# Kernel optimization log

Hardware: AMD Instinct MI355X
Metric: run time of the kernel (lower is better)

The kernel has to match this reference:

```python
import jax, jax.numpy as jnp
import numpy as np

EPS = 2.220446049250313e-16  # sys.float_info.epsilon
H_BW = 0.1  # bandwidth h


def setup_inputs() -> dict:
    key = jax.random.key(0)
    k1, k2 = jax.random.split(key)
    X = jax.random.normal(k1, (4, 256, 64, 64), dtype=jnp.float32)
    Y = jax.random.normal(k2, (4, 256, 64, 64), dtype=jnp.float32)
    return {"X_features": X, "Y_features": Y}


def _l2_normalize_c(f):
    # torch.norm(f, 2, dim=1, keepdim=True) + eps over channel dim of NCHW
    n = jnp.sqrt(jnp.sum(f * f, axis=1, keepdims=True)) + EPS
    return f / n


def reference(X_features, Y_features):
    B, C = X_features.shape[0], X_features.shape[1]
    # PONO centering: mean over channel dim of Y
    y_mean = jnp.mean(Y_features, axis=1, keepdims=True)  # [B,1,H,W]
    X = X_features - y_mean
    Y = Y_features - y_mean
    Xn = _l2_normalize_c(X).reshape(B, C, -1)  # [B,C,M]
    Yn = _l2_normalize_c(Y).reshape(B, C, -1)  # [B,C,M]
    # cosine distance matrix [B,M,M]
    d = 1.0 - jnp.einsum('bci,bcj->bij', Xn, Yn)
    d_norm = d / (jnp.min(d, axis=-1, keepdims=True) + 0.001)
    w = jnp.exp((1.0 - d_norm) / H_BW)
    A_ij = w / jnp.sum(w, axis=-1, keepdims=True)
    CX = jnp.mean(jnp.max(A_ij, axis=-1), axis=1)  # [B]
    return jnp.mean(-jnp.log(CX))
```

## Files before the change

### kernel.cpp

```cpp
#include <hip/hip_runtime.h>
#include <hip/hip_bf16.h>

typedef unsigned short u16;
typedef unsigned int u32;
typedef __attribute__((ext_vector_type(8))) __bf16 bf16x8;
typedef __attribute__((ext_vector_type(4))) float f32x4;
typedef __attribute__((ext_vector_type(8))) short short8;

#define EPSF 2.220446049250313e-16f

__device__ __forceinline__ u16 f2bf(float f) {
    u32 u = __float_as_uint(f);
    return (u16)((u + 0x7FFFu + ((u >> 16) & 1u)) >> 16);
}

__device__ __forceinline__ void gll16(const void* g, void* l) {
    __builtin_amdgcn_global_load_lds(
        (const __attribute__((address_space(1))) unsigned int*)g,
        (__attribute__((address_space(3))) unsigned int*)l, 16, 0, 0);
}

#define MEMFENCE asm volatile("" ::: "memory")
#define BAR() do { MEMFENCE; __builtin_amdgcn_s_barrier(); MEMFENCE; } while (0)
#define VMWAIT(N) do { asm volatile("s_waitcnt vmcnt(" #N ")" ::: "memory"); \
                       __builtin_amdgcn_sched_barrier(0); } while (0)

__global__ __launch_bounds__(512) void prep_kernel(
    const float* __restrict__ X, const float* __restrict__ Y,
    u16* __restrict__ XnT, u16* __restrict__ YnT)
{
    const int b  = blockIdx.x >> 7;
    const int p0 = (blockIdx.x & 127) << 5;
    const int t  = threadIdx.x;
    const int w  = t >> 6, l = t & 63;
    const size_t base = (size_t)b * 256 * 4096 + p0;

    __shared__ float TXf[32][260], TYf[32][260];
    __shared__ float part[8][16][8];
    __shared__ float meanL[32], rxL[32], ryL[32];

    const int pxp = t & 15;
    const int cs  = t >> 4;
    float sx0=0,sxx0=0,sy0=0,syy0=0, sx1=0,sxx1=0,sy1=0,syy1=0;
    #pragma unroll
    for (int k = 0; k < 8; ++k) {
        int c = cs * 8 + k;
        size_t off = base + (size_t)c * 4096 + pxp * 2;
        float2 vx = *(const float2*)(X + off);
        float2 vy = *(const float2*)(Y + off);
        TXf[pxp*2][c] = vx.x; TXf[pxp*2+1][c] = vx.y;
        TYf[pxp*2][c] = vy.x; TYf[pxp*2+1][c] = vy.y;
        sx0 += vx.x; sxx0 += vx.x*vx.x; sy0 += vy.x; syy0 += vy.x*vy.x;
        sx1 += vx.y; sxx1 += vx.y*vx.y; sy1 += vy.y; syy1 += vy.y*vy.y;
    }
    #pragma unroll
    for (int sh = 16; sh <= 32; sh <<= 1) {
        sx0 += __shfl_xor(sx0, sh, 64); sxx0 += __shfl_xor(sxx0, sh, 64);
        sy0 += __shfl_xor(sy0, sh, 64); syy0 += __shfl_xor(syy0, sh, 64);
        sx1 += __shfl_xor(sx1, sh, 64); sxx1 += __shfl_xor(sxx1, sh, 64);
        sy1 += __shfl_xor(sy1, sh, 64); syy1 += __shfl_xor(syy1, sh, 64);
    }
    if (l < 16) {
        part[w][l][0]=sx0; part[w][l][1]=sxx0; part[w][l][2]=sy0; part[w][l][3]=syy0;
        part[w][l][4]=sx1; part[w][l][5]=sxx1; part[w][l][6]=sy1; part[w][l][7]=syy1;
    }
    __syncthreads();
    if (t < 32) {
        const int pp = t >> 1, sub = (t & 1) * 4;
        float Sx=0, Sxx=0, Sy=0, Syy=0;
        #pragma unroll
        for (int ww = 0; ww < 8; ++ww) {
            Sx += part[ww][pp][sub+0]; Sxx += part[ww][pp][sub+1];
            Sy += part[ww][pp][sub+2]; Syy += part[ww][pp][sub+3];
        }
        float m = Sy * (1.f / 256.f);
        float ssx = fmaxf(Sxx - 2.f*m*Sx + 256.f*m*m, 0.f);
        float ssy = fmaxf(Syy - 2.f*m*Sy + 256.f*m*m, 0.f);
        meanL[t] = m;
        rxL[t] = 1.f / (sqrtf(ssx) + EPSF);
        ryL[t] = 1.f / (sqrtf(ssy) + EPSF);
    }
    __syncthreads();
    {
        const int c16 = t & 15, px = t >> 4;
        const float m = meanL[px], rxv = rxL[px], ryv = ryL[px];
        size_t ob = ((size_t)b * 4096 + p0 + px) * 256 + c16 * 16;
        #pragma unroll
        for (int h = 0; h < 2; ++h) {
            short8 hx, hy;
            #pragma unroll
            for (int k = 0; k < 8; ++k) {
                int c = c16 * 16 + h * 8 + k;
                hx[k] = (short)f2bf((TXf[px][c] - m) * rxv);
                hy[k] = (short)f2bf((TYf[px][c] - m) * ryv);
            }
            *(short8*)(XnT + ob + h * 8) = hx;
            *(short8*)(YnT + ob + h * 8) = hy;
        }
    }
}

template <int PASS>
__global__ __launch_bounds__(512, 2) void cx_pass(
    const u16* __restrict__ XnT, const u16* __restrict__ YnT,
    const float* __restrict__ smax, float* __restrict__ partials)
{
    __shared__ u16 As[2][2][128 * 64];
    __shared__ u16 Bs[2][2][128 * 64];
    __shared__ float red[256][4];
    __shared__ float smx[256];

    const int t = threadIdx.x;
    const int w = t >> 6;
    const int l = t & 63;
    const int wr  = w >> 2;
    const int wcn = w & 3;

    const int id   = blockIdx.x;
    const int xcd  = id & 7;
    const int slot = id >> 3;
    const int b    = xcd >> 1;
    const int tile = ((xcd & 1) << 7) | slot;
    const int it = tile >> 4, jt = tile & 15;
    const int i0 = it << 8, j0 = jt << 8;

    const u16* Ab = XnT + ((size_t)b * 4096 + i0) * 256;
    const u16* Bb = YnT + ((size_t)b * 4096 + j0) * 256;

    if (PASS == 1 && t < 256)
        smx[t] = smax[(size_t)b * 4096 + i0 + t];

    const int srow = t >> 3;
    const int sOff = srow * 256 + (((t & 7) ^ (srow & 7)) << 3);

    auto stageA = [&](int d, int h, int kt) {
        gll16(Ab + h * 32768 +         kt * 64 + sOff, &As[d][h][w * 512]);
        gll16(Ab + h * 32768 + 16384 + kt * 64 + sOff, &As[d][h][4096 + w * 512]);
    };
    auto stageB = [&](int d, int h, int kt) {
        gll16(Bb + h * 32768 +         kt * 64 + sOff, &Bs[d][h][w * 512]);
        gll16(Bb + h * 32768 + 16384 + kt * 64 + sOff, &Bs[d][h][4096 + w * 512]);
    };

    bf16x8 a[4][2], b0[2][2], b1[2][2];
    f32x4 acc[8][4] = {};

    const int l15 = l & 15;
    const int kbh = (l >> 4) << 4;

    auto readA = [&](int d, int mh) {
        const char* basep = (const char*)&As[d][wr][0];
        #pragma unroll
        for (int fm = 0; fm < 4; ++fm)
            #pragma unroll
            for (int ks = 0; ks < 2; ++ks) {
                int row = mh * 64 + fm * 16 + l15;
                int kb = ks * 64 + kbh;
                a[fm][ks] = *(const bf16x8*)(basep + row * 128 + (kb ^ ((row & 7) << 4)));
            }
    };
    auto readB = [&](int d, int nh, bf16x8 (&bb)[2][2]) {
        const char* basep = (const char*)&Bs[d][wcn >> 1][0];
        #pragma unroll
        for (int fp = 0; fp < 2; ++fp)
            #pragma unroll
            for (int ks = 0; ks < 2; ++ks) {
                int row = (wcn & 1) * 64 + (nh * 2 + fp) * 16 + l15;
                int kb = ks * 64 + kbh;
                bb[fp][ks] = *(const bf16x8*)(basep + row * 128 + (kb ^ ((row & 7) << 4)));
            }
    };
    auto mmaQ = [&](int mh, int nh, bf16x8 (&bb)[2][2]) {
        __builtin_amdgcn_s_setprio(1);
        #pragma unroll
        for (int fm = 0; fm < 4; ++fm)
            #pragma unroll
            for (int fp = 0; fp < 2; ++fp)
                #pragma unroll
                for (int ks = 0; ks < 2; ++ks)
                    acc[mh*4+fm][nh*2+fp] = __builtin_amdgcn_mfma_f32_16x16x32_bf16(
                        a[fm][ks], bb[fp][ks], acc[mh*4+fm][nh*2+fp], 0, 0, 0);
        __builtin_amdgcn_s_setprio(0);
    };

    stageA(0,0,0); stageA(0,1,0); stageB(0,0,0); stageB(0,1,0);
    stageA(1,0,1); stageA(1,1,1); stageB(1,0,1); stageB(1,1,1);

    VMWAIT(8); BAR();
    readA(0,0); readB(0,0,b0);  BAR(); mmaQ(0,0,b0);
    readB(0,1,b1);              BAR(); mmaQ(0,1,b1);
    readA(0,1);                 BAR(); mmaQ(1,1,b1);
    stageB(0,0,2);              BAR(); mmaQ(1,0,b0);
    VMWAIT(2); BAR();
    readA(1,0); readB(1,0,b0); stageB(0,1,2); BAR(); mmaQ(0,0,b0);
    readB(1,1,b1);             stageA(0,0,2); BAR(); mmaQ(0,1,b1);
    readA(1,1);                stageA(0,1,2); BAR(); mmaQ(1,1,b1);
    stageB(1,0,3);                            BAR(); mmaQ(1,0,b0);
    VMWAIT(2); BAR();
    readA(0,0); readB(0,0,b0); stageB(1,1,3); BAR(); mmaQ(0,0,b0);
    readB(0,1,b1);             stageA(1,0,3); BAR(); mmaQ(0,1,b1);
    readA(0,1);                stageA(1,1,3); BAR(); mmaQ(1,1,b1);
    BAR(); mmaQ(1,0,b0);
    VMWAIT(0); BAR();
    readA(1,0); readB(1,0,b0);  BAR(); mmaQ(0,0,b0);
    readB(1,1,b1);              BAR(); mmaQ(0,1,b1);
    readA(1,1);                 BAR(); mmaQ(1,1,b1);
    BAR(); mmaQ(1,0,b0);

    const int g = l >> 4;
    #pragma unroll
    for (int fm = 0; fm < 8; ++fm) {
        #pragma unroll
        for (int r = 0; r < 4; ++r) {
            const int rowL = wr * 128 + fm * 16 + g * 4 + r;
            float v;
            if (PASS == 0) {
                v = fmaxf(fmaxf(acc[fm][0][r], acc[fm][1][r]),
                          fmaxf(acc[fm][2][r], acc[fm][3][r]));
                v = fmaxf(v, __shfl_xor(v, 1, 64));
                v = fmaxf(v, __shfl_xor(v, 2, 64));
                v = fmaxf(v, __shfl_xor(v, 4, 64));
                v = fmaxf(v, __shfl_xor(v, 8, 64));
            } else {
                float mrow = smx[rowL];
                float itau = 1.0f / (0.1f * (1.001f - mrow));
                v = __expf((acc[fm][0][r] - mrow) * itau)
                  + __expf((acc[fm][1][r] - mrow) * itau)
                  + __expf((acc[fm][2][r] - mrow) * itau)
                  + __expf((acc[fm][3][r] - mrow) * itau);
                v += __shfl_xor(v, 1, 64);
                v += __shfl_xor(v, 2, 64);
                v += __shfl_xor(v, 4, 64);
                v += __shfl_xor(v, 8, 64);
            }
            if (l15 == 0) red[rowL][wcn] = v;
        }
    }
    BAR();
    if (t < 256) {
        float4 vv = *(const float4*)&red[t][0];
        float res = (PASS == 0)
            ? fmaxf(fmaxf(vv.x, vv.y), fmaxf(vv.z, vv.w))
            : (vv.x + vv.y) + (vv.z + vv.w);
        partials[((size_t)b * 4096 + i0 + t) * 16 + jt] = res;
    }
}

template <int OP>
__global__ __launch_bounds__(256) void reduce_rows(
    const float* __restrict__ part, float* __restrict__ outv)
{
    const int row = blockIdx.x * 256 + threadIdx.x;
    const float4* p = (const float4*)(part + (size_t)row * 16);
    float a = (OP == 0) ? -2.0f : 0.0f;
    #pragma unroll
    for (int k = 0; k < 4; ++k) {
        float4 v = p[k];
        if (OP == 0) a = fmaxf(a, fmaxf(fmaxf(v.x, v.y), fmaxf(v.z, v.w)));
        else         a += (v.x + v.y) + (v.z + v.w);
    }
    outv[row] = a;
}

__global__ __launch_bounds__(1024) void final_kernel(
    const float* __restrict__ Stot, float* __restrict__ out)
{
    __shared__ float red[16];
    const int t = threadIdx.x;
    float loss = 0.f;
    for (int b = 0; b < 4; ++b) {
        float s = 0.f;
        #pragma unroll
        for (int k = 0; k < 4; ++k)
            s += 1.0f / Stot[(size_t)b * 4096 + k * 1024 + t];
        #pragma unroll
        for (int sh = 1; sh <= 32; sh <<= 1) s += __shfl_xor(s, sh, 64);
        if ((t & 63) == 0) red[t >> 6] = s;
        __syncthreads();
        if (t == 0) {
            float tot = 0.f;
            #pragma unroll
            for (int k = 0; k < 16; ++k) tot += red[k];
            loss += -logf(tot * (1.f / 4096.f));
        }
        __syncthreads();
    }
    if (t == 0) out[0] = loss * 0.25f;
}

extern "C" void kernel_launch(void* const* d_in, const int* in_sizes, int n_in,
                              void* d_out, int out_size, void* d_ws, size_t ws_size,
                              hipStream_t stream)
{
    const float* X = (const float*)d_in[0];
    const float* Y = (const float*)d_in[1];
    char* ws = (char*)d_ws;
    u16* XnT = (u16*)(ws);
    u16* YnT = (u16*)(ws + (8u << 20));
    float* partials = (float*)(ws + (16u << 20));
    float* smax = (float*)(ws + (17u << 20));
    float* Stot = (float*)(ws + (17u << 20) + (64u << 10));
    float* out = (float*)d_out;

    hipLaunchKernelGGL(prep_kernel, dim3(512), dim3(512), 0, stream,
                       X, Y, XnT, YnT);
    hipLaunchKernelGGL((cx_pass<0>), dim3(1024), dim3(512), 0, stream,
                       XnT, YnT, smax, partials);
    hipLaunchKernelGGL((reduce_rows<0>), dim3(64), dim3(256), 0, stream,
                       partials, smax);
    hipLaunchKernelGGL((cx_pass<1>), dim3(1024), dim3(512), 0, stream,
                       XnT, YnT, smax, partials);
    hipLaunchKernelGGL((reduce_rows<1>), dim3(64), dim3(256), 0, stream,
                       partials, Stot);
    hipLaunchKernelGGL(final_kernel, dim3(1), dim3(1024), 0, stream, Stot, out);
}
```

Baseline: 200.5 us.

## Restructure CX passes into A-in-register tiles streaming long B row ranges

Each cx_pass block now keeps its 128-row A slice entirely in registers and streams 1024 B rows through a double-buffered LDS tile, accumulating the row max or exp-sum across the whole range. This cuts the column-tile partial count from 16 to 4, shrinks reduce_rows, and uses exp2 with a precomputed FMA offset. The prep kernel also gets odd-stride LDS padding and a remapped write pattern to reduce bank conflicts. The risks are higher register pressure from holding A fragments, fewer and smaller blocks (512 of 256 threads), and lower MFMA density per B load.

```diff
diff --git a/kernel.cpp b/kernel.cpp
--- a/kernel.cpp
+++ b/kernel.cpp
@@ -35,7 +35,7 @@
     const int w  = t >> 6, l = t & 63;
     const size_t base = (size_t)b * 256 * 4096 + p0;
 
-    __shared__ float TXf[32][260], TYf[32][260];
+    __shared__ float TXf[32 * 261], TYf[32 * 261];
     __shared__ float part[8][16][8];
     __shared__ float meanL[32], rxL[32], ryL[32];
 
@@ -48,8 +48,8 @@
         size_t off = base + (size_t)c * 4096 + pxp * 2;
         float2 vx = *(const float2*)(X + off);
         float2 vy = *(const float2*)(Y + off);
-        TXf[pxp*2][c] = vx.x; TXf[pxp*2+1][c] = vx.y;
-        TYf[pxp*2][c] = vy.x; TYf[pxp*2+1][c] = vy.y;
+        TXf[(pxp*2) * 261 + c] = vx.x; TXf[(pxp*2+1) * 261 + c] = vx.y;
+        TYf[(pxp*2) * 261 + c] = vy.x; TYf[(pxp*2+1) * 261 + c] = vy.y;
         sx0 += vx.x; sxx0 += vx.x*vx.x; sy0 += vy.x; syy0 += vy.x*vy.x;
         sx1 += vx.y; sxx1 += vx.y*vx.y; sy1 += vy.y; syy1 += vy.y*vy.y;
     }
@@ -82,17 +82,17 @@
     }
     __syncthreads();
     {
-        const int c16 = t & 15, px = t >> 4;
+        const int px = t & 31, cb = t >> 5;
         const float m = meanL[px], rxv = rxL[px], ryv = ryL[px];
-        size_t ob = ((size_t)b * 4096 + p0 + px) * 256 + c16 * 16;
+        size_t ob = ((size_t)b * 4096 + p0 + px) * 256 + cb * 16;
         #pragma unroll
         for (int h = 0; h < 2; ++h) {
             short8 hx, hy;
             #pragma unroll
             for (int k = 0; k < 8; ++k) {
-                int c = c16 * 16 + h * 8 + k;
-                hx[k] = (short)f2bf((TXf[px][c] - m) * rxv);
-                hy[k] = (short)f2bf((TYf[px][c] - m) * ryv);
+                int c = cb * 16 + h * 8 + k;
+                hx[k] = (short)f2bf((TXf[px * 261 + c] - m) * rxv);
+                hy[k] = (short)f2bf((TYf[px * 261 + c] - m) * ryv);
             }
             *(short8*)(XnT + ob + h * 8) = hx;
             *(short8*)(YnT + ob + h * 8) = hy;
@@ -101,149 +101,135 @@
 }
 
 template <int PASS>
-__global__ __launch_bounds__(512, 2) void cx_pass(
+__global__ __launch_bounds__(256, 2) void cx_pass(
     const u16* __restrict__ XnT, const u16* __restrict__ YnT,
     const float* __restrict__ smax, float* __restrict__ partials)
 {
-    __shared__ u16 As[2][2][128 * 64];
-    __shared__ u16 Bs[2][2][128 * 64];
-    __shared__ float red[256][4];
-    __shared__ float smx[256];
+    __shared__ u16 Bs[2][16384];
 
     const int t = threadIdx.x;
     const int w = t >> 6;
     const int l = t & 63;
-    const int wr  = w >> 2;
-    const int wcn = w & 3;
+    const int l15 = l & 15, g = l >> 4;
 
     const int id   = blockIdx.x;
     const int xcd  = id & 7;
     const int slot = id >> 3;
     const int b    = xcd >> 1;
-    const int tile = ((xcd & 1) << 7) | slot;
-    const int it = tile >> 4, jt = tile & 15;
-    const int i0 = it << 8, j0 = jt << 8;
+    const int tid2 = ((xcd & 1) << 6) | slot;
+    const int it = tid2 >> 2, jr = tid2 & 3;
+    const int i0 = it << 7;
+    const int j0 = jr << 10;
 
     const u16* Ab = XnT + ((size_t)b * 4096 + i0) * 256;
     const u16* Bb = YnT + ((size_t)b * 4096 + j0) * 256;
 
-    if (PASS == 1 && t < 256)
-        smx[t] = smax[(size_t)b * 4096 + i0 + t];
-
-    const int srow = t >> 3;
-    const int sOff = srow * 256 + (((t & 7) ^ (srow & 7)) << 3);
-
-    auto stageA = [&](int d, int h, int kt) {
-        gll16(Ab + h * 32768 +         kt * 64 + sOff, &As[d][h][w * 512]);
-        gll16(Ab + h * 32768 + 16384 + kt * 64 + sOff, &As[d][h][4096 + w * 512]);
+    bf16x8 a[2][8];
+    #pragma unroll
+    for (int fm = 0; fm < 2; ++fm)
+        #pragma unroll
+        for (int ks = 0; ks < 8; ++ks)
+            a[fm][ks] = *(const bf16x8*)((const char*)Ab +
+                (size_t)(w * 32 + fm * 16 + l15) * 512 + ks * 64 + g * 16);
+
+    float moff[2][4], itau[2][4];
+    if (PASS == 1) {
+        #pragma unroll
+        for (int fm = 0; fm < 2; ++fm)
+            #pragma unroll
+            for (int r = 0; r < 4; ++r) {
+                float m = smax[(size_t)b * 4096 + i0 + w * 32 + fm * 16 + g * 4 + r];
+                float itv = 1.44269504f / (0.1f * (1.001f - m));
+                itau[fm][r] = itv;
+                moff[fm][r] = m * itv;
+            }
+    }
+
+    const int srow0 = t >> 5;
+    const int gch   = ((t & 31) ^ srow0);
+    auto stage = [&](int d, int st) {
+        const u16* Bt = Bb + (size_t)st * 64 * 256;
+        #pragma unroll
+        for (int q = 0; q < 8; ++q)
+            gll16(Bt + (size_t)(q * 8 + srow0) * 256 + gch * 8,
+                  &Bs[d][q * 2048 + w * 512]);
     };
-    auto stageB = [&](int d, int h, int kt) {
-        gll16(Bb + h * 32768 +         kt * 64 + sOff, &Bs[d][h][w * 512]);
-        gll16(Bb + h * 32768 + 16384 + kt * 64 + sOff, &Bs[d][h][4096 + w * 512]);
-    };
-
-    bf16x8 a[4][2], b0[2][2], b1[2][2];
-    f32x4 acc[8][4] = {};
-
-    const int l15 = l & 15;
-    const int kbh = (l >> 4) << 4;
-
-    auto readA = [&](int d, int mh) {
-        const char* basep = (const char*)&As[d][wr][0];
-        #pragma unroll
-        for (int fm = 0; fm < 4; ++fm)
-            #pragma unroll
-            for (int ks = 0; ks < 2; ++ks) {
-                int row = mh * 64 + fm * 16 + l15;
-                int kb = ks * 64 + kbh;
-                a[fm][ks] = *(const bf16x8*)(basep + row * 128 + (kb ^ ((row & 7) << 4)));
-            }
-    };
-    auto readB = [&](int d, int nh, bf16x8 (&bb)[2][2]) {
-        const char* basep = (const char*)&Bs[d][wcn >> 1][0];
-        #pragma unroll
-        for (int fp = 0; fp < 2; ++fp)
-            #pragma unroll
-            for (int ks = 0; ks < 2; ++ks) {
-                int row = (wcn & 1) * 64 + (nh * 2 + fp) * 16 + l15;
-                int kb = ks * 64 + kbh;
-                bb[fp][ks] = *(const bf16x8*)(basep + row * 128 + (kb ^ ((row & 7) << 4)));
-            }
-    };
-    auto mmaQ = [&](int mh, int nh, bf16x8 (&bb)[2][2]) {
-        __builtin_amdgcn_s_setprio(1);
-        #pragma unroll
-        for (int fm = 0; fm < 4; ++fm)
-            #pragma unroll
-            for (int fp = 0; fp < 2; ++fp)
+
+    float racc[2][4];
+    #pragma unroll
+    for (int fm = 0; fm < 2; ++fm)
+        #pragma unroll
+        for (int r = 0; r < 4; ++r) racc[fm][r] = (PASS == 0) ? -2.0f : 0.0f;
+
+    const int bswz = (l15 & 7) << 4;
+
+    stage(0, 0);
+
+    #pragma unroll
+    for (int s = 0; s < 16; ++s) {
+        if (s < 15) stage((s + 1) & 1, s + 1);
+        if (s < 15) { VMWAIT(8); } else { VMWAIT(0); }
+        BAR();
+        {
+            const char* bp = (const char*)&Bs[s & 1][0];
+            f32x4 acc[2][4] = {};
+            #pragma unroll
+            for (int ks = 0; ks < 8; ++ks) {
+                bf16x8 bf[4];
                 #pragma unroll
-                for (int ks = 0; ks < 2; ++ks)
-                    acc[mh*4+fm][nh*2+fp] = __builtin_amdgcn_mfma_f32_16x16x32_bf16(
-                        a[fm][ks], bb[fp][ks], acc[mh*4+fm][nh*2+fp], 0, 0, 0);
-        __builtin_amdgcn_s_setprio(0);
-    };
-
-    stageA(0,0,0); stageA(0,1,0); stageB(0,0,0); stageB(0,1,0);
-    stageA(1,0,1); stageA(1,1,1); stageB(1,0,1); stageB(1,1,1);
-
-    VMWAIT(8); BAR();
-    readA(0,0); readB(0,0,b0);  BAR(); mmaQ(0,0,b0);
-    readB(0,1,b1);              BAR(); mmaQ(0,1,b1);
-    readA(0,1);                 BAR(); mmaQ(1,1,b1);
-    stageB(0,0,2);              BAR(); mmaQ(1,0,b0);
-    VMWAIT(2); BAR();
-    readA(1,0); readB(1,0,b0); stageB(0,1,2); BAR(); mmaQ(0,0,b0);
-    readB(1,1,b1);             stageA(0,0,2); BAR(); mmaQ(0,1,b1);
-    readA(1,1);                stageA(0,1,2); BAR(); mmaQ(1,1,b1);
-    stageB(1,0,3);                            BAR(); mmaQ(1,0,b0);
-    VMWAIT(2); BAR();
-    readA(0,0); readB(0,0,b0); stageB(1,1,3); BAR(); mmaQ(0,0,b0);
-    readB(0,1,b1);             stageA(1,0,3); BAR(); mmaQ(0,1,b1);
-    readA(0,1);                stageA(1,1,3); BAR(); mmaQ(1,1,b1);
-    BAR(); mmaQ(1,0,b0);
-    VMWAIT(0); BAR();
-    readA(1,0); readB(1,0,b0);  BAR(); mmaQ(0,0,b0);
-    readB(1,1,b1);              BAR(); mmaQ(0,1,b1);
-    readA(1,1);                 BAR(); mmaQ(1,1,b1);
-    BAR(); mmaQ(1,0,b0);
-
-    const int g = l >> 4;
-    #pragma unroll
-    for (int fm = 0; fm < 8; ++fm) {
+                for (int fn = 0; fn < 4; ++fn) {
+                    int row = fn * 16 + l15;
+                    bf[fn] = *(const bf16x8*)(bp + row * 512 +
+                                              ((ks * 64 + g * 16) ^ bswz));
+                }
+                __builtin_amdgcn_s_setprio(1);
+                #pragma unroll
+                for (int fm = 0; fm < 2; ++fm)
+                    #pragma unroll
+                    for (int fn = 0; fn < 4; ++fn)
+                        acc[fm][fn] = __builtin_amdgcn_mfma_f32_16x16x32_bf16(
+                            a[fm][ks], bf[fn], acc[fm][fn], 0, 0, 0);
+                __builtin_amdgcn_s_setprio(0);
+            }
+            #pragma unroll
+            for (int fm = 0; fm < 2; ++fm)
+                #pragma unroll
+                for (int r = 0; r < 4; ++r) {
+                    if (PASS == 0) {
+                        float v = fmaxf(fmaxf(acc[fm][0][r], acc[fm][1][r]),
+                                        fmaxf(acc[fm][2][r], acc[fm][3][r]));
+                        racc[fm][r] = fmaxf(racc[fm][r], v);
+                    } else {
+                        float e0 = exp2f(fmaf(acc[fm][0][r], itau[fm][r], -moff[fm][r]));
+                        float e1 = exp2f(fmaf(acc[fm][1][r], itau[fm][r], -moff[fm][r]));
+                        float e2 = exp2f(fmaf(acc[fm][2][r], itau[fm][r], -moff[fm][r]));
+                        float e3 = exp2f(fmaf(acc[fm][3][r], itau[fm][r], -moff[fm][r]));
+                        racc[fm][r] += (e0 + e1) + (e2 + e3);
+                    }
+                }
+        }
+        BAR();
+    }
+
+    #pragma unroll
+    for (int fm = 0; fm < 2; ++fm)
         #pragma unroll
         for (int r = 0; r < 4; ++r) {
-            const int rowL = wr * 128 + fm * 16 + g * 4 + r;
-            float v;
+            float v = racc[fm][r];
             if (PASS == 0) {
-                v = fmaxf(fmaxf(acc[fm][0][r], acc[fm][1][r]),
-                          fmaxf(acc[fm][2][r], acc[fm][3][r]));
                 v = fmaxf(v, __shfl_xor(v, 1, 64));
                 v = fmaxf(v, __shfl_xor(v, 2, 64));
                 v = fmaxf(v, __shfl_xor(v, 4, 64));
                 v = fmaxf(v, __shfl_xor(v, 8, 64));
             } else {
-                float mrow = smx[rowL];
-                float itau = 1.0f / (0.1f * (1.001f - mrow));
-                v = __expf((acc[fm][0][r] - mrow) * itau)
-                  + __expf((acc[fm][1][r] - mrow) * itau)
-                  + __expf((acc[fm][2][r] - mrow) * itau)
-                  + __expf((acc[fm][3][r] - mrow) * itau);
                 v += __shfl_xor(v, 1, 64);
                 v += __shfl_xor(v, 2, 64);
                 v += __shfl_xor(v, 4, 64);
                 v += __shfl_xor(v, 8, 64);
             }
-            if (l15 == 0) red[rowL][wcn] = v;
-        }
-    }
-    BAR();
-    if (t < 256) {
-        float4 vv = *(const float4*)&red[t][0];
-        float res = (PASS == 0)
-            ? fmaxf(fmaxf(vv.x, vv.y), fmaxf(vv.z, vv.w))
-            : (vv.x + vv.y) + (vv.z + vv.w);
-        partials[((size_t)b * 4096 + i0 + t) * 16 + jt] = res;
-    }
+            if (l15 == 0)
+                partials[((size_t)b * 4096 + i0 + w * 32 + fm * 16 + g * 4 + r) * 4 + jr] = v;
+        }
 }
 
 template <int OP>
@@ -251,15 +237,10 @@
     const float* __restrict__ part, float* __restrict__ outv)
 {
     const int row = blockIdx.x * 256 + threadIdx.x;
-    const float4* p = (const float4*)(part + (size_t)row * 16);
-    float a = (OP == 0) ? -2.0f : 0.0f;
-    #pragma unroll
-    for (int k = 0; k < 4; ++k) {
-        float4 v = p[k];
-        if (OP == 0) a = fmaxf(a, fmaxf(fmaxf(v.x, v.y), fmaxf(v.z, v.w)));
-        else         a += (v.x + v.y) + (v.z + v.w);
-    }
-    outv[row] = a;
+    float4 v = *(const float4*)(part + (size_t)row * 4);
+    outv[row] = (OP == 0)
+        ? fmaxf(fmaxf(v.x, v.y), fmaxf(v.z, v.w))
+        : (v.x + v.y) + (v.z + v.w);
 }
 
 __global__ __launch_bounds__(1024) void final_kernel(
@@ -304,11 +285,11 @@
 
     hipLaunchKernelGGL(prep_kernel, dim3(512), dim3(512), 0, stream,
                        X, Y, XnT, YnT);
-    hipLaunchKernelGGL((cx_pass<0>), dim3(1024), dim3(512), 0, stream,
+    hipLaunchKernelGGL((cx_pass<0>), dim3(512), dim3(256), 0, stream,
                        XnT, YnT, smax, partials);
     hipLaunchKernelGGL((reduce_rows<0>), dim3(64), dim3(256), 0, stream,
                        partials, smax);
-    hipLaunchKernelGGL((cx_pass<1>), dim3(1024), dim3(512), 0, stream,
+    hipLaunchKernelGGL((cx_pass<1>), dim3(512), dim3(256), 0, stream,
                        XnT, YnT, smax, partials);
     hipLaunchKernelGGL((reduce_rows<1>), dim3(64), dim3(256), 0, stream,
                        partials, Stot);
```

Measured after the change: 272.1 us. 35.7% more time.
